# Kernel tuning notes

Measured on AMD Instinct MI355X. Metric: run time of the kernel, lower is better.

Reference implementation:

```python
import jax, jax.numpy as jnp
import numpy as np
from jax import lax

B, C_IN, C_OUT, H, W, K = 32, 128, 256, 56, 56, 3
STRIDE, PAD = 1, 1
LAMBDA_C, LAMBDA_A = 0.0, 1.0  # adaptive_weights=False defaults


def setup_inputs() -> dict:
    key = jax.random.key(0)
    k1, k2, k3 = jax.random.split(key, 3)
    x = jax.random.normal(k1, (B, C_IN, H, W), dtype=jnp.float32)
    weight = jax.random.normal(k2, (C_OUT, C_IN, K, K), dtype=jnp.float32) * 0.05
    bias = jax.random.normal(k3, (C_OUT,), dtype=jnp.float32) * 0.05
    return {"x": x, "weight": weight, "bias": bias}


def reference(x, weight, bias):
    # For each k x k patch X and kernel slice Kc (per in-channel):
    #   sum(X@Kc) = sum_{a,c} X[a,c] * rowsum(Kc)[c]   (depends on patch column index)
    #   sum(Kc@X) = sum_{c,b} X[c,b] * colsum(Kc)[c]   (depends on patch row index)
    # So lambda_c*(XK-KX).sum() + lambda_a*(XK+KX).sum() summed over in-channels is
    # exactly a conv2d with the effective kernel below.
    krow = weight.sum(axis=3)  # [O, I, k]  rowsum: sum over last kernel axis
    kcol = weight.sum(axis=2)  # [O, I, k]  colsum: sum over first kernel axis
    # W_eff[o,i,r,s] = (la+lc)*krow[o,i,s] + (la-lc)*kcol[o,i,r]
    w_eff = (LAMBDA_A + LAMBDA_C) * krow[:, :, None, :] \
          + (LAMBDA_A - LAMBDA_C) * kcol[:, :, :, None]
    y = lax.conv_general_dilated(
        x, w_eff,
        window_strides=(STRIDE, STRIDE),
        padding=[(PAD, PAD), (PAD, PAD)],
        dimension_numbers=("NCHW", "OIHW", "NCHW"),
    )
    return y + bias[None, :, None, None]
```

## Files before the change

### kernel.cpp

```cpp
#include <hip/hip_runtime.h>
#include <hip/hip_fp16.h>
#include <stdint.h>

typedef unsigned short u16;
typedef _Float16 half8 __attribute__((ext_vector_type(8)));
typedef float floatx4 __attribute__((ext_vector_type(4)));

#define B_N 32
#define CI  128
#define CO  256
#define HH  56
#define WW  56
#define HP  58
#define WP  58

static const size_t XP_OFF = 590080;
static const size_t XP_SZ  = (size_t)32 * 58 * 7424 * 2;
static const size_t XV_OFF = XP_OFF + XP_SZ;
static const size_t XV_SZ  = (size_t)32 * 56 * 7424 * 2;
static const size_t XH_OFF = XV_OFF + XV_SZ;
static const size_t XH_SZ  = (size_t)32 * 58 * 7168 * 2;
static const size_t WS_NEED = XH_OFF + XH_SZ + 1024;

__device__ __forceinline__ float bf2f(u16 u) {
  union { uint32_t i; float f; } c; c.i = ((uint32_t)u) << 16; return c.f;
}
__device__ __forceinline__ u16 f2bf(float f) {
  union { float f; uint32_t i; } c; c.f = f;
  uint32_t u = c.i;
  u += 0x7fffu + ((u >> 16) & 1u);
  return (u16)(u >> 16);
}
__device__ __forceinline__ u16 f2h16(float f) {
  __half h = __float2half_rn(f);
  return *reinterpret_cast<u16*>(&h);
}
__device__ __forceinline__ uint32_t pack2h(float a, float b) {
  __half2 h = __floats2half2_rn(a, b);
  return *reinterpret_cast<uint32_t*>(&h);
}
__device__ __forceinline__ int4 add3(int4 a, int4 b, int4 c) {
  __half2* pa = (__half2*)&a; __half2* pb = (__half2*)&b; __half2* pc = (__half2*)&c;
  int4 r; __half2* pr = (__half2*)&r;
#pragma unroll
  for (int i = 0; i < 4; ++i) pr[i] = __hadd2(__hadd2(pa[i], pb[i]), pc[i]);
  return r;
}

__device__ __forceinline__ bool detect_bf16(const void* __restrict__ bias) {
  int lane = threadIdx.x & 63;
  float a = fabsf(bf2f(((const u16*)bias)[lane]));
  bool plausible = (a >= 1e-5f) && (a <= 0.5f);
  unsigned long long m = __ballot(plausible);
  return __popcll(m) >= 50;
}

__global__ __launch_bounds__(256) void k_prep(const void* __restrict__ xsrc,
                                              const void* __restrict__ wsrc,
                                              u16* __restrict__ xp,
                                              u16* __restrict__ wb,
                                              const void* __restrict__ bias) {
  const int hp = blockIdx.x, b = blockIdx.y, tid = threadIdx.x;
  if (hp == HP) {
    const bool isbf = detect_bf16(bias);
#pragma unroll 1
    for (int sub = 0; sub < 4; ++sub) {
      int t = (b * 4 + sub) * 256 + tid;
      float v[9];
      if (isbf) {
        const u16* p = (const u16*)wsrc + (size_t)t * 9;
#pragma unroll
        for (int j = 0; j < 9; ++j) v[j] = bf2f(p[j]);
      } else {
        const float* p = (const float*)wsrc + (size_t)t * 9;
#pragma unroll
        for (int j = 0; j < 9; ++j) v[j] = p[j];
      }
      float rowsum[3] = { v[0]+v[1]+v[2], v[3]+v[4]+v[5], v[6]+v[7]+v[8] };
      float colsum[3] = { v[0]+v[3]+v[6], v[1]+v[4]+v[7], v[2]+v[5]+v[8] };
      const int o = t >> 7, i = t & 127;
      const int osub = o >> 4, lo = o & 15;
      const int ic = i >> 5, q = (i >> 3) & 3, j = i & 7;
#pragma unroll
      for (int s = 0; s < 3; ++s) {
        int k = s * 4 + ic;
        wb[((size_t)(k * 16 + osub) * 64 + q * 16 + lo) * 8 + j] = f2h16(rowsum[s]);
      }
#pragma unroll
      for (int r = 0; r < 3; ++r) {
        int k = 12 + r * 4 + ic;
        wb[((size_t)(k * 16 + osub) * 64 + q * 16 + lo) * 8 + j] = f2h16(colsum[r]);
      }
    }
    return;
  }
  __shared__ uint32_t tile32[CI * 29];
  u16* dst = xp + (size_t)(b * HP + hp) * (16 * WP * 8);
  if (hp == 0 || hp == HP - 1) {
    int4 z = {0, 0, 0, 0};
    for (int c = tid; c < 928; c += 256) *(int4*)(dst + c * 8) = z;
    return;
  }
  const bool isbf = detect_bf16(bias);
  const int h = hp - 1;
  if (isbf) {
    const uint32_t* xr = (const uint32_t*)xsrc;
    for (int c = tid; c < CI * 28; c += 256) {
      int i = c / 28, wp = c - i * 28;
      uint32_t p2 = xr[((size_t)(b * CI + i) * HH + h) * 28 + wp];
      tile32[i * 29 + wp] = pack2h(bf2f((u16)p2), bf2f((u16)(p2 >> 16)));
    }
  } else {
    const float4* xr = (const float4*)xsrc;
    for (int c = tid; c < CI * 14; c += 256) {
      int i = c / 14, f4 = c - i * 14;
      float4 v = xr[((size_t)(b * CI + i) * HH + h) * 14 + f4];
      tile32[i * 29 + 2 * f4]     = pack2h(v.x, v.y);
      tile32[i * 29 + 2 * f4 + 1] = pack2h(v.z, v.w);
    }
  }
  __syncthreads();
  const u16* t16 = (const u16*)tile32;
  uint32_t* dw = (uint32_t*)dst;
  for (int c = tid; c < 16 * 56 * 4; c += 256) {
    int g = c / 224, rem = c - g * 224, w = rem >> 2, jj = rem & 3;
    int i0 = g * 8 + jj * 2;
    uint32_t lo16 = t16[i0 * 58 + w], hi16 = t16[(i0 + 1) * 58 + w];
    dw[(g * 58 + (w + 1)) * 4 + jj] = lo16 | (hi16 << 16);
  }
  if (tid < 128) {
    int g = tid >> 3, k = tid & 7, wb_ = (k >> 2) * 57, jj = k & 3;
    dw[(g * 58 + wb_) * 4 + jj] = 0;
  }
}

__global__ __launch_bounds__(256) void k_box(const u16* __restrict__ xp,
                                             u16* __restrict__ xh) {
  const int u = blockIdx.x, b = blockIdx.y, tid = threadIdx.x;
  const int4* r0 = (const int4*)(xp + (size_t)(b * HP + u) * 7424);
  int4* hd = (int4*)(xh + (size_t)(b * HP + u) * 7168);
  for (int c = tid; c < 16 * 56; c += 256) {
    int g = c / 56, w = c - g * 56;
    const int4* s = r0 + g * 58 + w;
    hd[c] = add3(s[0], s[1], s[2]);
  }
}

#define GSTRIDE 472
#define RSTRIDE (16 * 472)

#define ALOAD(BUF, K)                                                       \
  {                                                                         \
    const u16* ap = wb + ((size_t)((K)*16 + osubbase) << 9) + lane * 8;     \
    af[BUF][0] = *(const half8*)ap;                                         \
    af[BUF][1] = *(const half8*)(ap + 512);                                 \
    af[BUF][2] = *(const half8*)(ap + 1024);                                \
    af[BUF][3] = *(const half8*)(ap + 1536);                                \
  }
#define MSTEP(BUF)                                                          \
  _Pragma("unroll") for (int m = 0; m < 4; ++m)                             \
      _Pragma("unroll") for (int n = 0; n < 8; ++n) acc[m][n] =             \
          __builtin_amdgcn_mfma_f32_16x16x32_f16(af[BUF][m], bfr[BUF][n],   \
                                                 acc[m][n], 0, 0, 0);

#define BLOAD(BUF, K)                                                       \
  {                                                                         \
    int ic_ = (K)&3;                                                        \
    int t_, co_;                                                            \
    if ((K) < 12) { t_ = 2 * rp;                    co_ = (lo + ((K) >> 2)) * 8; } \
    else          { t_ = 4 + 2 * rp + (((K)-12) >> 2); co_ = lo * 8; }      \
    const u16* bp = Bs + ((t_ * 16 + ic_ * 4 + quad) * GSTRIDE) + co_;      \
    bfr[BUF][0] = *(const half8*)bp;                                        \
    bfr[BUF][1] = *(const half8*)(bp + 128);                                \
    bfr[BUF][2] = *(const half8*)(bp + 256);                                \
    bfr[BUF][3] = *(const half8*)(bp + 384);                                \
    bfr[BUF][4] = *(const half8*)(bp + RSTRIDE);                            \
    bfr[BUF][5] = *(const half8*)(bp + RSTRIDE + 128);                      \
    bfr[BUF][6] = *(const half8*)(bp + RSTRIDE + 256);                      \
    bfr[BUF][7] = *(const half8*)(bp + RSTRIDE + 384);                      \
  }

__global__ __launch_bounds__(512, 2) void k_gemm(const u16* __restrict__ wb,
                                                 const u16* __restrict__ xp,
                                                 const void* __restrict__ bias,
                                                 void* __restrict__ outv) {
  __shared__ u16 Bs[10 * RSTRIDE + 64];
  const int lin = blockIdx.y * (HH / 4) + blockIdx.x;
  const int swz = (lin & 7) * (448 / 8) + (lin >> 3);
  const int b = swz / (HH / 4);
  const int p0 = 4 * (swz - b * (HH / 4));
  const int tid = threadIdx.x;
  const int wv = tid >> 6, lane = tid & 63;
  const int lo = lane & 15, quad = lane >> 4;
  const int aq = wv & 3, rp = wv >> 2;
  const int osubbase = aq * 4;

  {
    const u16* xb = xp + (size_t)(b * HP) * 7424;
    for (int c = tid; c < 4 * 928; c += 512) {
      int t = c / 928, rem = c - t * 928;
      const int4* src = (const int4*)(xb + (size_t)(p0 + t) * 7424) + rem;
      int g = rem / 58, w = rem - g * 58;
      *(int4*)(Bs + (size_t)((t * 16 + g) * 59 + w) * 8) =
          add3(src[0], src[928], src[1856]);
    }
    for (int c = tid; c < 6 * 896; c += 512) {
      int u = c / 896, rem = c - u * 896;
      int g = rem / 56, w = rem - g * 56;
      const int4* src = (const int4*)(xb + (size_t)(p0 + u) * 7424) + g * 58 + w;
      *(int4*)(Bs + (size_t)(((4 + u) * 16 + g) * 59 + w) * 8) =
          add3(src[0], src[1], src[2]);
    }
    if (tid < 192) {
      int u = tid / 32, rem = tid - u * 32, g = rem >> 1, w = 56 + (rem & 1);
      *(int4*)(Bs + (size_t)(((4 + u) * 16 + g) * 59 + w) * 8) = (int4){0, 0, 0, 0};
    }
  }
  __syncthreads();

  floatx4 acc[4][8];
#pragma unroll
  for (int m = 0; m < 4; ++m)
#pragma unroll
    for (int n = 0; n < 8; ++n) acc[m][n] = (floatx4){0.f, 0.f, 0.f, 0.f};

  half8 af[2][4], bfr[2][8];
  ALOAD(0, 0); BLOAD(0, 0);
#pragma unroll 1
  for (int k = 0; k < 24; k += 2) {
    ALOAD(1, k + 1); BLOAD(1, k + 1);
    MSTEP(0);
    if (k + 2 < 24) { ALOAD(0, k + 2); BLOAD(0, k + 2); }
    MSTEP(1);
  }

  const bool isbf = detect_bf16(bias);
  const int prow = p0 + 2 * rp;
  if (isbf) {
    u16* out = (u16*)outv;
    const u16* bs = (const u16*)bias;
#pragma unroll
    for (int m = 0; m < 4; ++m)
#pragma unroll
      for (int v = 0; v < 4; ++v) {
        const int o = aq * 64 + m * 16 + quad * 4 + v;
        const float bv = bf2f(bs[o]);
        size_t base = ((size_t)(b * CO + o) * HH + prow) * WW;
#pragma unroll
        for (int n = 0; n < 8; ++n) {
          const int q = (n & 3) * 16 + lo;
          if (q < WW) out[base + (n >> 2) * WW + q] = f2bf(acc[m][n][v] + bv);
        }
      }
  } else {
    float* out = (float*)outv;
    const float* bs = (const float*)bias;
#pragma unroll
    for (int m = 0; m < 4; ++m)
#pragma unroll
      for (int v = 0; v < 4; ++v) {
        const int o = aq * 64 + m * 16 + quad * 4 + v;
        const float bv = bs[o];
        size_t base = ((size_t)(b * CO + o) * HH + prow) * WW;
#pragma unroll
        for (int n = 0; n < 8; ++n) {
          const int q = (n & 3) * 16 + lo;
          if (q < WW) out[base + (n >> 2) * WW + q] = acc[m][n][v] + bv;
        }
      }
  }
}

#define BLOAD_H(BUF, K)                                                     \
  {                                                                         \
    const int ic_ = (K)&3;                                                  \
    const u16* bp; size_t rstr;                                             \
    if ((K) < 12) {                                                         \
      bp = Bs + ((ic_ * 4 + quad) * GSTRIDE) + (lo + ((K) >> 2)) * 8;       \
      rstr = RSTRIDE;                                                       \
    } else {                                                                \
      bp = xh + ((size_t)((b * HP + p0 + (((K)-12) >> 2)) * 16 + ic_ * 4 + quad)) * 448 + lo * 8; \
      rstr = 7168;                                                          \
    }                                                                       \
    bfr[BUF][0] = *(const half8*)bp;                                        \
    bfr[BUF][1] = *(const half8*)(bp + 128);                                \
    bfr[BUF][2] = *(const half8*)(bp + 256);                                \
    bfr[BUF][3] = *(const half8*)(bp + 384);                                \
    bfr[BUF][4] = *(const half8*)(bp + rstr);                               \
    bfr[BUF][5] = *(const half8*)(bp + rstr + 128);                        \
    bfr[BUF][6] = *(const half8*)(bp + rstr + 256);                        \
    bfr[BUF][7] = *(const half8*)(bp + rstr + 384);                        \
  }

__global__ __launch_bounds__(256, 2) void k_gemm_h(const u16* __restrict__ wb,
                                                   const u16* __restrict__ xp,
                                                   const u16* __restrict__ xh,
                                                   const void* __restrict__ bias,
                                                   void* __restrict__ outv) {
  __shared__ u16 Bs[2 * RSTRIDE + 64];
  const int lin = blockIdx.y * (HH / 2) + blockIdx.x;
  const int swz = (lin & 7) * 112 + (lin >> 3);
  const int b = swz / (HH / 2);
  const int p0 = 2 * (swz - b * (HH / 2));
  const int tid = threadIdx.x;
  const int wv = tid >> 6, lane = tid & 63;
  const int lo = lane & 15, quad = lane >> 4;
  const int osubbase = wv * 4;

  {
    const u16* xb = xp + (size_t)(b * HP) * 7424;
    for (int c = tid; c < 2 * 928; c += 256) {
      int t = c >> 9 >= 1 ? c / 928 : 0;
      t = c / 928;
      int rem = c - t * 928;
      const int4* src = (const int4*)(xb + (size_t)(p0 + t) * 7424) + rem;
      int g = rem / 58, w = rem - g * 58;
      *(int4*)(Bs + (size_t)((t * 16 + g) * 59 + w) * 8) =
          add3(src[0], src[928], src[1856]);
    }
  }
  __syncthreads();

  floatx4 acc[4][8];
#pragma unroll
  for (int m = 0; m < 4; ++m)
#pragma unroll
    for (int n = 0; n < 8; ++n) acc[m][n] = (floatx4){0.f, 0.f, 0.f, 0.f};

  half8 af[2][4], bfr[2][8];
  ALOAD(0, 0); BLOAD_H(0, 0);
#pragma unroll 1
  for (int k = 0; k < 24; k += 2) {
    ALOAD(1, k + 1); BLOAD_H(1, k + 1);
    MSTEP(0);
    if (k + 2 < 24) { ALOAD(0, k + 2); BLOAD_H(0, k + 2); }
    MSTEP(1);
  }

  const bool isbf = detect_bf16(bias);
  if (isbf) {
    u16* out = (u16*)outv;
    const u16* bs = (const u16*)bias;
#pragma unroll
    for (int m = 0; m < 4; ++m)
#pragma unroll
      for (int v = 0; v < 4; ++v) {
        const int o = wv * 64 + m * 16 + quad * 4 + v;
        const float bv = bf2f(bs[o]);
        size_t base = ((size_t)(b * CO + o) * HH + p0) * WW;
#pragma unroll
        for (int n = 0; n < 8; ++n) {
          const int q = (n & 3) * 16 + lo;
          if (q < WW) out[base + (n >> 2) * WW + q] = f2bf(acc[m][n][v] + bv);
        }
      }
  } else {
    float* out = (float*)outv;
    const float* bs = (const float*)bias;
#pragma unroll
    for (int m = 0; m < 4; ++m)
#pragma unroll
      for (int v = 0; v < 4; ++v) {
        const int o = wv * 64 + m * 16 + quad * 4 + v;
        const float bv = bs[o];
        size_t base = ((size_t)(b * CO + o) * HH + p0) * WW;
#pragma unroll
        for (int n = 0; n < 8; ++n) {
          const int q = (n & 3) * 16 + lo;
          if (q < WW) out[base + (n >> 2) * WW + q] = acc[m][n][v] + bv;
        }
      }
  }
}

extern "C" void kernel_launch(void* const* d_in, const int* in_sizes, int n_in,
                              void* d_out, int out_size, void* d_ws, size_t ws_size,
                              hipStream_t stream) {
  const void* x    = d_in[0];
  const void* w    = d_in[1];
  const void* bias = d_in[2];
  uint8_t* ws = (uint8_t*)d_ws;
  u16* wb = (u16*)ws;
  u16* xp = (u16*)(ws + XP_OFF);

  k_prep<<<dim3(HP + 1, B_N), 256, 0, stream>>>(x, w, xp, wb, bias);
  if (ws_size >= WS_NEED) {
    u16* xh = (u16*)(ws + XH_OFF);
    k_box<<<dim3(HP, B_N), 256, 0, stream>>>(xp, xh);
    k_gemm_h<<<dim3(HH / 2, B_N), 256, 0, stream>>>(wb, xp, xh, bias, d_out);
  } else {
    k_gemm<<<dim3(HH / 4, B_N), 512, 0, stream>>>(wb, xp, bias, d_out);
  }
}
```

Baseline: 204.1 us.

## Fuse horizontal box-sum into prep kernel and switch GEMM to 32x32 MFMA

```diff
diff --git a/kernel.cpp b/kernel.cpp
--- a/kernel.cpp
+++ b/kernel.cpp
@@ -5,6 +5,7 @@
 typedef unsigned short u16;
 typedef _Float16 half8 __attribute__((ext_vector_type(8)));
 typedef float floatx4 __attribute__((ext_vector_type(4)));
+typedef float floatx16 __attribute__((ext_vector_type(16)));
 
 #define B_N 32
 #define CI  128
@@ -16,9 +17,7 @@
 
 static const size_t XP_OFF = 590080;
 static const size_t XP_SZ  = (size_t)32 * 58 * 7424 * 2;
-static const size_t XV_OFF = XP_OFF + XP_SZ;
-static const size_t XV_SZ  = (size_t)32 * 56 * 7424 * 2;
-static const size_t XH_OFF = XV_OFF + XV_SZ;
+static const size_t XH_OFF = XP_OFF + XP_SZ;
 static const size_t XH_SZ  = (size_t)32 * 58 * 7168 * 2;
 static const size_t WS_NEED = XH_OFF + XH_SZ + 1024;
 
@@ -58,6 +57,7 @@
 __global__ __launch_bounds__(256) void k_prep(const void* __restrict__ xsrc,
                                               const void* __restrict__ wsrc,
                                               u16* __restrict__ xp,
+                                              u16* __restrict__ xh,
                                               u16* __restrict__ wb,
                                               const void* __restrict__ bias) {
   const int hp = blockIdx.x, b = blockIdx.y, tid = threadIdx.x;
@@ -95,14 +95,17 @@
     return;
   }
   __shared__ uint32_t tile32[CI * 29];
-  u16* dst = xp + (size_t)(b * HP + hp) * (16 * WP * 8);
+  u16* dst  = xp + (size_t)(b * HP + hp) * (16 * WP * 8);
+  u16* dsth = xh + (size_t)(b * HP + hp) * 7168;
   if (hp == 0 || hp == HP - 1) {
     int4 z = {0, 0, 0, 0};
     for (int c = tid; c < 928; c += 256) *(int4*)(dst + c * 8) = z;
+    for (int c = tid; c < 896; c += 256) *(int4*)(dsth + c * 8) = z;
     return;
   }
   const bool isbf = detect_bf16(bias);
   const int h = hp - 1;
+  if (tid < 128) tile32[tid * 29 + 28] = 0;
   if (isbf) {
     const uint32_t* xr = (const uint32_t*)xsrc;
     for (int c = tid; c < CI * 28; c += 256) {
@@ -132,17 +135,21 @@
     int g = tid >> 3, k = tid & 7, wb_ = (k >> 2) * 57, jj = k & 3;
     dw[(g * 58 + wb_) * 4 + jj] = 0;
   }
-}
-
-__global__ __launch_bounds__(256) void k_box(const u16* __restrict__ xp,
-                                             u16* __restrict__ xh) {
-  const int u = blockIdx.x, b = blockIdx.y, tid = threadIdx.x;
-  const int4* r0 = (const int4*)(xp + (size_t)(b * HP + u) * 7424);
-  int4* hd = (int4*)(xh + (size_t)(b * HP + u) * 7168);
-  for (int c = tid; c < 16 * 56; c += 256) {
-    int g = c / 56, w = c - g * 56;
-    const int4* s = r0 + g * 58 + w;
-    hd[c] = add3(s[0], s[1], s[2]);
+  {
+    const __half* ha = (const __half*)t16;
+    uint32_t* hw = (uint32_t*)dsth;
+    for (int c = tid; c < 16 * 56 * 4; c += 256) {
+      int g = c / 224, rem = c - g * 224, q = rem >> 2, jj = rem & 3;
+      int r0 = (g * 8 + jj * 2) * 58, r1 = r0 + 58;
+      __half zl = __float2half_rn(0.f);
+      __half s0 = (q ? ha[r0 + q - 1] : zl);
+      __half s1 = (q ? ha[r1 + q - 1] : zl);
+      __half lo = __hadd(__hadd(s0, ha[r0 + q]), ha[r0 + q + 1]);
+      __half hi = __hadd(__hadd(s1, ha[r1 + q]), ha[r1 + q + 1]);
+      hw[(g * 56 + q) * 4 + jj] =
+          (uint32_t)*reinterpret_cast<u16*>(&lo) |
+          ((uint32_t)*reinterpret_cast<u16*>(&hi) << 16);
+    }
   }
 }
 
@@ -157,12 +164,6 @@
     af[BUF][2] = *(const half8*)(ap + 1024);                                \
     af[BUF][3] = *(const half8*)(ap + 1536);                                \
   }
-#define MSTEP(BUF)                                                          \
-  _Pragma("unroll") for (int m = 0; m < 4; ++m)                             \
-      _Pragma("unroll") for (int n = 0; n < 8; ++n) acc[m][n] =             \
-          __builtin_amdgcn_mfma_f32_16x16x32_f16(af[BUF][m], bfr[BUF][n],   \
-                                                 acc[m][n], 0, 0, 0);
-
 #define BLOAD(BUF, K)                                                       \
   {                                                                         \
     int ic_ = (K)&3;                                                        \
@@ -179,6 +180,11 @@
     bfr[BUF][6] = *(const half8*)(bp + RSTRIDE + 256);                      \
     bfr[BUF][7] = *(const half8*)(bp + RSTRIDE + 384);                      \
   }
+#define MSTEP(BUF)                                                          \
+  _Pragma("unroll") for (int m = 0; m < 4; ++m)                             \
+      _Pragma("unroll") for (int n = 0; n < 8; ++n) acc[m][n] =             \
+          __builtin_amdgcn_mfma_f32_16x16x32_f16(af[BUF][m], bfr[BUF][n],   \
+                                                 acc[m][n], 0, 0, 0);
 
 __global__ __launch_bounds__(512, 2) void k_gemm(const u16* __restrict__ wb,
                                                  const u16* __restrict__ xp,
@@ -271,48 +277,70 @@
   }
 }
 
-#define BLOAD_H(BUF, K)                                                     \
+#define ALOAD32(BUF, K)                                                     \
+  {                                                                         \
+    const int mo_ = (lane & 31) >> 4;                                       \
+    const u16* ap = wb + ((size_t)(((K)*16 + osubbase + mo_) * 64) + hq16) * 8; \
+    af[BUF][0] = *(const half8*)ap;                                         \
+    af[BUF][1] = *(const half8*)(ap + 256);       \
+    af[BUF][2] = *(const half8*)(ap + 1024);      \
+    af[BUF][3] = *(const half8*)(ap + 1280);                                \
+  }
+#define BLOAD32(BUF, K)                                                     \
   {                                                                         \
     const int ic_ = (K)&3;                                                  \
-    const u16* bp; size_t rstr;                                             \
     if ((K) < 12) {                                                         \
-      bp = Bs + ((ic_ * 4 + quad) * GSTRIDE) + (lo + ((K) >> 2)) * 8;       \
-      rstr = RSTRIDE;                                                       \
+      const int s_ = (K) >> 2;                                              \
+      const u16* bp = Bs + (ic_ * 4 + hi2) * GSTRIDE + (s_ + l31) * 8;      \
+      bfr[BUF][0] = *(const half8*)bp;                                      \
+      bfr[BUF][1] = *(const half8*)(bp + 2 * GSTRIDE);                      \
+      bfr[BUF][2] = *(const half8*)(bp + 256);                              \
+      bfr[BUF][3] = *(const half8*)(bp + 2 * GSTRIDE + 256);                \
+      bfr[BUF][4] = *(const half8*)(bp + RSTRIDE);                          \
+      bfr[BUF][5] = *(const half8*)(bp + RSTRIDE + 2 * GSTRIDE);            \
+      bfr[BUF][6] = *(const half8*)(bp + RSTRIDE + 256);                    \
+      bfr[BUF][7] = *(const half8*)(bp + RSTRIDE + 2 * GSTRIDE + 256);      \
     } else {                                                                \
-      bp = xh + ((size_t)((b * HP + p0 + (((K)-12) >> 2)) * 16 + ic_ * 4 + quad)) * 448 + lo * 8; \
-      rstr = 7168;                                                          \
+      const int r_ = ((K)-12) >> 2;                                         \
+      const u16* bp = xh + ((size_t)((b * HP + p0 + r_) * 16 + ic_ * 4 + hi2)) * 448 + l31 * 8; \
+      bfr[BUF][0] = *(const half8*)bp;                                      \
+      bfr[BUF][1] = *(const half8*)(bp + 2 * 448);                          \
+      bfr[BUF][2] = *(const half8*)(bp + 256);                              \
+      bfr[BUF][3] = *(const half8*)(bp + 2 * 448 + 256);                    \
+      bfr[BUF][4] = *(const half8*)(bp + 7168);                             \
+      bfr[BUF][5] = *(const half8*)(bp + 7168 + 2 * 448);                   \
+      bfr[BUF][6] = *(const half8*)(bp + 7168 + 256);                       \
+      bfr[BUF][7] = *(const half8*)(bp + 7168 + 2 * 448 + 256);             \
     }                                                                       \
-    bfr[BUF][0] = *(const half8*)bp;                                        \
-    bfr[BUF][1] = *(const half8*)(bp + 128);                                \
-    bfr[BUF][2] = *(const half8*)(bp + 256);                                \
-    bfr[BUF][3] = *(const half8*)(bp + 384);                                \
-    bfr[BUF][4] = *(const half8*)(bp + rstr);                               \
-    bfr[BUF][5] = *(const half8*)(bp + rstr + 128);                        \
-    bfr[BUF][6] = *(const half8*)(bp + rstr + 256);                        \
-    bfr[BUF][7] = *(const half8*)(bp + rstr + 384);                        \
-  }
-
-__global__ __launch_bounds__(256, 2) void k_gemm_h(const u16* __restrict__ wb,
-                                                   const u16* __restrict__ xp,
-                                                   const u16* __restrict__ xh,
-                                                   const void* __restrict__ bias,
-                                                   void* __restrict__ outv) {
-  __shared__ u16 Bs[2 * RSTRIDE + 64];
+  }
+#define MSTEP32(BUF)                                                        \
+  _Pragma("unroll") for (int h = 0; h < 2; ++h)                             \
+      _Pragma("unroll") for (int m = 0; m < 2; ++m)                         \
+          _Pragma("unroll") for (int nf = 0; nf < 4; ++nf) acc[m][nf] =     \
+              __builtin_amdgcn_mfma_f32_32x32x16_f16(af[BUF][m*2+h],        \
+                  bfr[BUF][nf*2+h], acc[m][nf], 0, 0, 0);
+
+__global__ __launch_bounds__(256, 2) void k_gemm_h32(const u16* __restrict__ wb,
+                                                     const u16* __restrict__ xp,
+                                                     const u16* __restrict__ xh,
+                                                     const void* __restrict__ bias,
+                                                     void* __restrict__ outv) {
+  __shared__ u16 Bs[2 * RSTRIDE + 80];
   const int lin = blockIdx.y * (HH / 2) + blockIdx.x;
   const int swz = (lin & 7) * 112 + (lin >> 3);
   const int b = swz / (HH / 2);
   const int p0 = 2 * (swz - b * (HH / 2));
   const int tid = threadIdx.x;
   const int wv = tid >> 6, lane = tid & 63;
-  const int lo = lane & 15, quad = lane >> 4;
+  const int l31 = lane & 31, hi5 = lane >> 5;
+  const int hi2 = hi5;
+  const int hq16 = hi5 * 16 + (lane & 15);
   const int osubbase = wv * 4;
 
   {
     const u16* xb = xp + (size_t)(b * HP) * 7424;
     for (int c = tid; c < 2 * 928; c += 256) {
-      int t = c >> 9 >= 1 ? c / 928 : 0;
-      t = c / 928;
-      int rem = c - t * 928;
+      int t = c / 928, rem = c - t * 928;
       const int4* src = (const int4*)(xb + (size_t)(p0 + t) * 7424) + rem;
       int g = rem / 58, w = rem - g * 58;
       *(int4*)(Bs + (size_t)((t * 16 + g) * 59 + w) * 8) =
@@ -321,20 +349,22 @@
   }
   __syncthreads();
 
-  floatx4 acc[4][8];
-#pragma unroll
-  for (int m = 0; m < 4; ++m)
-#pragma unroll
-    for (int n = 0; n < 8; ++n) acc[m][n] = (floatx4){0.f, 0.f, 0.f, 0.f};
+  floatx16 acc[2][4];
+#pragma unroll
+  for (int m = 0; m < 2; ++m)
+#pragma unroll
+    for (int nf = 0; nf < 4; ++nf)
+#pragma unroll
+      for (int v = 0; v < 16; ++v) acc[m][nf][v] = 0.f;
 
   half8 af[2][4], bfr[2][8];
-  ALOAD(0, 0); BLOAD_H(0, 0);
+  ALOAD32(0, 0); BLOAD32(0, 0);
 #pragma unroll 1
   for (int k = 0; k < 24; k += 2) {
-    ALOAD(1, k + 1); BLOAD_H(1, k + 1);
-    MSTEP(0);
-    if (k + 2 < 24) { ALOAD(0, k + 2); BLOAD_H(0, k + 2); }
-    MSTEP(1);
+    ALOAD32(1, k + 1); BLOAD32(1, k + 1);
+    MSTEP32(0);
+    if (k + 2 < 24) { ALOAD32(0, k + 2); BLOAD32(0, k + 2); }
+    MSTEP32(1);
   }
 
   const bool isbf = detect_bf16(bias);
@@ -342,32 +372,32 @@
     u16* out = (u16*)outv;
     const u16* bs = (const u16*)bias;
 #pragma unroll
-    for (int m = 0; m < 4; ++m)
-#pragma unroll
-      for (int v = 0; v < 4; ++v) {
-        const int o = wv * 64 + m * 16 + quad * 4 + v;
+    for (int m = 0; m < 2; ++m)
+#pragma unroll
+      for (int v = 0; v < 16; ++v) {
+        const int o = wv * 64 + m * 32 + (v & 3) + 8 * (v >> 2) + 4 * hi5;
         const float bv = bf2f(bs[o]);
         size_t base = ((size_t)(b * CO + o) * HH + p0) * WW;
 #pragma unroll
-        for (int n = 0; n < 8; ++n) {
-          const int q = (n & 3) * 16 + lo;
-          if (q < WW) out[base + (n >> 2) * WW + q] = f2bf(acc[m][n][v] + bv);
+        for (int nf = 0; nf < 4; ++nf) {
+          const int q = (nf & 1) * 32 + l31;
+          if (q < WW) out[base + (nf >> 1) * WW + q] = f2bf(acc[m][nf][v] + bv);
         }
       }
   } else {
     float* out = (float*)outv;
     const float* bs = (const float*)bias;
 #pragma unroll
-    for (int m = 0; m < 4; ++m)
-#pragma unroll
-      for (int v = 0; v < 4; ++v) {
-        const int o = wv * 64 + m * 16 + quad * 4 + v;
+    for (int m = 0; m < 2; ++m)
+#pragma unroll
+      for (int v = 0; v < 16; ++v) {
+        const int o = wv * 64 + m * 32 + (v & 3) + 8 * (v >> 2) + 4 * hi5;
         const float bv = bs[o];
         size_t base = ((size_t)(b * CO + o) * HH + p0) * WW;
 #pragma unroll
-        for (int n = 0; n < 8; ++n) {
-          const int q = (n & 3) * 16 + lo;
-          if (q < WW) out[base + (n >> 2) * WW + q] = acc[m][n][v] + bv;
+        for (int nf = 0; nf < 4; ++nf) {
+          const int q = (nf & 1) * 32 + l31;
+          if (q < WW) out[base + (nf >> 1) * WW + q] = acc[m][nf][v] + bv;
         }
       }
   }
@@ -382,12 +412,11 @@
   uint8_t* ws = (uint8_t*)d_ws;
   u16* wb = (u16*)ws;
   u16* xp = (u16*)(ws + XP_OFF);
-
-  k_prep<<<dim3(HP + 1, B_N), 256, 0, stream>>>(x, w, xp, wb, bias);
+  u16* xh = (u16*)(ws + XH_OFF);
+
+  k_prep<<<dim3(HP + 1, B_N), 256, 0, stream>>>(x, w, xp, xh, wb, bias);
   if (ws_size >= WS_NEED) {
-    u16* xh = (u16*)(ws + XH_OFF);
-    k_box<<<dim3(HP, B_N), 256, 0, stream>>>(xp, xh);
-    k_gemm_h<<<dim3(HH / 2, B_N), 256, 0, stream>>>(wb, xp, xh, bias, d_out);
+    k_gemm_h32<<<dim3(HH / 2, B_N), 256, 0, stream>>>(wb, xp, xh, bias, d_out);
   } else {
     k_gemm<<<dim3(HH / 4, B_N), 512, 0, stream>>>(wb, xp, bias, d_out);
   }
```

Result: slower. 215.4 us (+5.5%).
